# Performance work log

Measured on AMD Instinct MI355X. Metric: run time of the kernel, lower is better.

The kernel has to match this reference:

```python
import jax, jax.numpy as jnp
import numpy as np

B, L, IN_DIM = 256, 128, 6
D, H, NL = 256, 8, 6          # d_model, heads, wave layers
E, TOPK, FF = 8, 2, 1024      # MoE experts, top-k, expert ff dim (4*D)
NH, NMOE = 5, 3               # forecast horizons, MoE layers = NL//2
DK = D // H


def setup_inputs() -> dict:
    key = jax.random.key(0)
    ks = jax.random.split(key, 16)
    n = lambda k, shp, s=0.02: jax.random.normal(k, shp, dtype=jnp.float32) * s
    return dict(
        x=jax.random.normal(ks[0], (B, L, IN_DIM), dtype=jnp.float32),
        emb_w=n(ks[1], (IN_DIM, D)), emb_b=jnp.zeros((D,), jnp.float32),
        qw=n(ks[2], (NL, D, D)), kw=n(ks[3], (NL, D, D)),
        vw=n(ks[4], (NL, D, D)), ow=n(ks[5], (NL, D, D)),
        wfreq=n(ks[6], (NL, H), 0.1), wphase=jnp.zeros((NL, H), jnp.float32),
        router_w=n(ks[7], (NMOE, D, E)), router_b=jnp.zeros((NMOE, E), jnp.float32),
        e_w1=n(ks[8], (NMOE, E, D, FF)), e_b1=jnp.zeros((NMOE, E, FF), jnp.float32),
        e_w2=n(ks[9], (NMOE, E, FF, D)), e_b2=jnp.zeros((NMOE, E, D), jnp.float32),
        ln_g=jnp.ones((D,), jnp.float32), ln_b=jnp.zeros((D,), jnp.float32),
        pred_w=n(ks[10], (D, NH)), pred_b=jnp.zeros((NH,), jnp.float32),
        unc_w=n(ks[11], (D, NH)), unc_b=jnp.zeros((NH,), jnp.float32),
    )


def _wave_attn(x, qw, kw, vw, ow, freq, phase):
    # x: [B, L, D]; frequency-modulated multiplicative attention (dropout = eval)
    b, l, d = x.shape
    q = (x @ qw).reshape(b, l, H, DK).transpose(0, 2, 1, 3)  # [B,H,L,DK]
    k = (x @ kw).reshape(b, l, H, DK).transpose(0, 2, 1, 3)
    v = (x @ vw).reshape(b, l, H, DK).transpose(0, 2, 1, 3)
    pos = jnp.arange(l, dtype=x.dtype)
    wave = jnp.cos(2.0 * jnp.pi * freq[:, None] * pos[None, :] + phase[:, None])  # [H,L]
    scores = jnp.einsum('bhqd,bhkd->bhqk', q, k) * (DK ** -0.5)
    scores = scores * wave[None, :, None, :]
    attn = jax.nn.softmax(scores, axis=-1)
    out = jnp.einsum('bhqk,bhkd->bhqd', attn, v)
    out = out.transpose(0, 2, 1, 3).reshape(b, l, d)
    return out @ ow


def _moe(x, rw, rb, w1, b1, w2, b2):
    # x: [B, L, D] -> flatten tokens; top-k routed expert FFN with renormalized weights
    b, l, d = x.shape
    xf = x.reshape(-1, d)                                   # [N, D]
    probs = jax.nn.softmax(xf @ rw + rb, axis=-1)           # [N, E]
    tw, ti = jax.lax.top_k(probs, TOPK)                     # [N, K]
    tw = tw / jnp.sum(tw, axis=-1, keepdims=True)
    # combine weights per expert: nonzero only where expert is in token's top-k
    combine = jnp.sum(jax.nn.one_hot(ti, E, dtype=xf.dtype) * tw[..., None], axis=1)  # [N, E]
    out = jnp.zeros_like(xf)
    for e in range(E):  # fixed small expert count
        h = jax.nn.gelu(xf @ w1[e] + b1[e], approximate=False)
        out = out + combine[:, e:e + 1] * (h @ w2[e] + b2[e])
    return out.reshape(b, l, d)


def _forward(x, emb_w, emb_b, qw, kw, vw, ow, wfreq, wphase,
             router_w, router_b, e_w1, e_b1, e_w2, e_b2,
             ln_g, ln_b, pred_w, pred_b, unc_w, unc_b):
    h = x @ emb_w + emb_b
    for i in range(NL):
        h = _wave_attn(h, qw[i], kw[i], vw[i], ow[i], wfreq[i], wphase[i]) + h
        if i % 2 == 0 and i // 2 < NMOE:
            j = i // 2
            h = _moe(h, router_w[j], router_b[j], e_w1[j], e_b1[j], e_w2[j], e_b2[j]) + h
    mu = jnp.mean(h, axis=-1, keepdims=True)
    var = jnp.mean((h - mu) ** 2, axis=-1, keepdims=True)
    hn = (h - mu) / jnp.sqrt(var + 1e-5) * ln_g + ln_b
    z = hn[:, -1, :]                                        # last token latent
    pred = z @ pred_w + pred_b
    unc = jax.nn.softplus(z @ unc_w + unc_b)
    return pred, unc


def reference(x, emb_w, emb_b, qw, kw, vw, ow, wfreq, wphase,
              router_w, router_b, e_w1, e_b1, e_w2, e_b2,
              ln_g, ln_b, pred_w, pred_b, unc_w, unc_b):
    return _forward(x, emb_w, emb_b, qw, kw, vw, ow, wfreq, wphase,
                    router_w, router_b, e_w1, e_b1, e_w2, e_b2,
                    ln_g, ln_b, pred_w, pred_b, unc_w, unc_b)
```

## Files before the change

kernel.cpp:

```cpp
#include <hip/hip_runtime.h>
#include <math.h>

#define B_    256
#define L_    128
#define IN_   6
#define D_    256
#define H_    8
#define NL_   6
#define E_    8
#define FF_   1024
#define NH_   5
#define NMOE_ 3
#define DK_   32
#define T_    (B_*L_)
#define CAP_  66560

typedef __bf16 bf16x8 __attribute__((ext_vector_type(8)));
typedef __bf16 bf16x4 __attribute__((ext_vector_type(4)));
typedef float  f32x4  __attribute__((ext_vector_type(4)));

static constexpr size_t OFF_H    = 0;
static constexpr size_t OFF_HB   = 33554432;
static constexpr size_t OFF_QKV  = 50331648;
static constexpr size_t OFF_AO   = 100663296;
static constexpr size_t OFF_YOUT = 50331648;
static constexpr size_t OFF_WQKV = 118489088;
static constexpr size_t OFF_OWT  = 120848384;
static constexpr size_t OFF_W1T  = 121634816;
static constexpr size_t OFF_W2T  = 134217728;
static constexpr size_t OFF_SMALL= 146800640;
static constexpr size_t SM_T2I   = OFF_SMALL + 0;
static constexpr size_t SM_T2W   = OFF_SMALL + 262144;
static constexpr size_t SM_SLOT  = OFF_SMALL + 524288;
static constexpr size_t SM_PTOK  = OFF_SMALL + 786432;
static constexpr size_t SM_CNT   = OFF_SMALL + 1052672;
static constexpr size_t SM_POFF  = OFF_SMALL + 1052704;
static constexpr size_t SM_CUR   = OFF_SMALL + 1052740;

__global__ __launch_bounds__(256) void k_tcast(const float* __restrict__ src,
                                               __bf16* __restrict__ dst, int R, int C,
                                               size_t dbs, int rowoff) {
    __shared__ float tile[64][65];
    int b  = blockIdx.z;
    int r0 = blockIdx.y * 64, c0 = blockIdx.x * 64;
    const float* S = src + (size_t)b * R * C;
    __bf16* Dd = dst + (size_t)b * dbs;
    int tid = threadIdx.x;
#pragma unroll
    for (int i = 0; i < 4; ++i) {
        int f = tid + 256 * i;
        int r = f >> 4, c4 = (f & 15) * 4;
        float4 v = *(const float4*)(S + (size_t)(r0 + r) * C + c0 + c4);
        tile[r][c4] = v.x; tile[r][c4+1] = v.y; tile[r][c4+2] = v.z; tile[r][c4+3] = v.w;
    }
    __syncthreads();
#pragma unroll
    for (int i = 0; i < 2; ++i) {
        int chunk = tid + 256 * i;
        int drow = chunk >> 3, seg = (chunk & 7) * 8;
        bf16x8 o;
#pragma unroll
        for (int j = 0; j < 8; ++j) o[j] = (__bf16)tile[seg + j][drow];
        *(bf16x8*)(Dd + (size_t)(rowoff + c0 + drow) * R + r0 + seg) = o;
    }
}

__global__ void k_embed(const float* __restrict__ x, const float* __restrict__ ew,
                        const float* __restrict__ eb, float* __restrict__ h,
                        __bf16* __restrict__ hb) {
    int t = blockIdx.x;
    int d = threadIdx.x;
    const float* xr = x + (size_t)t * IN_;
    float acc = eb[d];
#pragma unroll
    for (int i = 0; i < IN_; ++i) acc = fmaf(xr[i], ew[i*D_ + d], acc);
    h[(size_t)t*D_ + d]  = acc;
    hb[(size_t)t*D_ + d] = (__bf16)acc;
}

#define LDT_ 40
__device__ __forceinline__ void mm_main(const __bf16* __restrict__ A, int lda,
                                        const __bf16* __restrict__ BT, int ldb,
                                        size_t m0, size_t n0, int K,
                                        f32x4 (&acc)[4][4],
                                        __bf16* As, __bf16* Bs) {
    const int tid  = threadIdx.x;
    const int lane = tid & 63, wid = tid >> 6;
    const int wm = (wid >> 1) * 64, wn = (wid & 1) * 64;
    const int lr = lane & 15, lq = lane >> 4;
    for (int k0 = 0; k0 < K; k0 += 32) {
#pragma unroll
        for (int i = 0; i < 2; ++i) {
            int f = tid + 256 * i;
            int row = f >> 2, q = (f & 3) * 8;
            *(bf16x8*)&As[row*LDT_ + q] = *(const bf16x8*)(A  + (m0 + row) * lda + k0 + q);
            *(bf16x8*)&Bs[row*LDT_ + q] = *(const bf16x8*)(BT + (n0 + row) * ldb + k0 + q);
        }
        __syncthreads();
        bf16x8 af[4], bfr[4];
#pragma unroll
        for (int mi = 0; mi < 4; ++mi) af[mi]  = *(bf16x8*)&As[(wm + mi*16 + lr)*LDT_ + lq*8];
#pragma unroll
        for (int ni = 0; ni < 4; ++ni) bfr[ni] = *(bf16x8*)&Bs[(wn + ni*16 + lr)*LDT_ + lq*8];
#pragma unroll
        for (int mi = 0; mi < 4; ++mi)
#pragma unroll
            for (int ni = 0; ni < 4; ++ni)
                acc[mi][ni] = __builtin_amdgcn_mfma_f32_16x16x32_bf16(af[mi], bfr[ni],
                                                                      acc[mi][ni], 0, 0, 0);
        __syncthreads();
    }
}

__global__ __launch_bounds__(256) void k_mm_c(const __bf16* __restrict__ A,
                                              const __bf16* __restrict__ BT,
                                              __bf16* __restrict__ C, int ldc) {
    __shared__ __attribute__((aligned(16))) __bf16 As[128*LDT_], Bs[128*LDT_];
    f32x4 acc[4][4] = {};
    size_t m0 = (size_t)blockIdx.x * 128, n0 = (size_t)blockIdx.y * 128;
    mm_main(A, D_, BT, D_, m0, n0, D_, acc, As, Bs);
    const int lane = threadIdx.x & 63, wid = threadIdx.x >> 6;
    const int wm = (wid >> 1) * 64, wn = (wid & 1) * 64, lr = lane & 15, lq = lane >> 4;
#pragma unroll
    for (int mi = 0; mi < 4; ++mi)
#pragma unroll
        for (int r = 0; r < 4; ++r) {
            size_t gr = m0 + wm + mi*16 + lq*4 + r;
#pragma unroll
            for (int ni = 0; ni < 4; ++ni) {
                size_t gc = n0 + wn + ni*16 + lr;
                C[gr * ldc + gc] = (__bf16)acc[mi][ni][r];
            }
        }
}

__global__ __launch_bounds__(256) void k_mm_oproj(const __bf16* __restrict__ A,
                                                  const __bf16* __restrict__ BT,
                                                  float* __restrict__ h,
                                                  __bf16* __restrict__ hb) {
    __shared__ __attribute__((aligned(16))) __bf16 As[128*LDT_], Bs[128*LDT_];
    f32x4 acc[4][4] = {};
    size_t m0 = (size_t)blockIdx.x * 128, n0 = (size_t)blockIdx.y * 128;
    mm_main(A, D_, BT, D_, m0, n0, D_, acc, As, Bs);
    const int lane = threadIdx.x & 63, wid = threadIdx.x >> 6;
    const int wm = (wid >> 1) * 64, wn = (wid & 1) * 64, lr = lane & 15, lq = lane >> 4;
#pragma unroll
    for (int mi = 0; mi < 4; ++mi)
#pragma unroll
        for (int r = 0; r < 4; ++r) {
            size_t gr = m0 + wm + mi*16 + lq*4 + r;
#pragma unroll
            for (int ni = 0; ni < 4; ++ni) {
                size_t gc = n0 + wn + ni*16 + lr;
                size_t idx = gr * D_ + gc;
                float nv = h[idx] + acc[mi][ni][r];
                h[idx]  = nv;
                hb[idx] = (__bf16)nv;
            }
        }
}

__global__ __launch_bounds__(256) void k_attn_mfma(const __bf16* __restrict__ qkv,
                                                   const float* __restrict__ wfreq,
                                                   const float* __restrict__ wphase,
                                                   __bf16* __restrict__ ao) {
    __shared__ __attribute__((aligned(16))) char smem[44032];
    __bf16* Vt   = (__bf16*)smem;
    float*  wscp = (float*)(smem + 8704);
    __bf16* Qs   = (__bf16*)(smem + 9216);
    __bf16* Ks   = (__bf16*)(smem + 19456);
    __bf16* Ps   = (__bf16*)(smem + 9216);

    int bh = blockIdx.x;
    int b = bh >> 3, hh = bh & 7;
    int tid = threadIdx.x;
    size_t tokbase = (size_t)b * L_ * 768 + (size_t)hh * 32;

#pragma unroll
    for (int j = 0; j < 2; ++j) {
        int chunk = tid + j*256;
        int row = chunk >> 2, seg = (chunk & 3) * 8;
        *(bf16x8*)&Qs[row*40 + seg] = *(const bf16x8*)(qkv + tokbase + (size_t)row*768 + seg);
        *(bf16x8*)&Ks[row*40 + seg] = *(const bf16x8*)(qkv + tokbase + 256 + (size_t)row*768 + seg);
    }
    {
        int kp = tid >> 1, dkb = (tid & 1) * 16;
        bf16x8 v0 = *(const bf16x8*)(qkv + tokbase + 512 + (size_t)kp*768 + dkb);
        bf16x8 v1 = *(const bf16x8*)(qkv + tokbase + 512 + (size_t)kp*768 + dkb + 8);
#pragma unroll
        for (int j = 0; j < 8; ++j) {
            Vt[(dkb + j)*136 + kp]     = v0[j];
            Vt[(dkb + 8 + j)*136 + kp] = v1[j];
        }
    }
    if (tid < 128) {
        float f = wfreq[hh], ph = wphase[hh];
        wscp[tid] = 0.1767766952966369f * cosf(6.283185307179586f * f * (float)tid + ph);
    }
    __syncthreads();

    const int lane = tid & 63, w = tid >> 6;
    const int lr = lane & 15, lq = lane >> 4;

    f32x4 sacc[2][8] = {};
#pragma unroll
    for (int mi = 0; mi < 2; ++mi) {
        bf16x8 af = *(const bf16x8*)&Qs[(w*32 + mi*16 + lr)*40 + lq*8];
#pragma unroll
        for (int ni = 0; ni < 8; ++ni) {
            bf16x8 bfr = *(const bf16x8*)&Ks[(ni*16 + lr)*40 + lq*8];
            sacc[mi][ni] = __builtin_amdgcn_mfma_f32_16x16x32_bf16(af, bfr, sacc[mi][ni], 0,0,0);
        }
    }
    float wr[8];
#pragma unroll
    for (int ni = 0; ni < 8; ++ni) wr[ni] = wscp[ni*16 + lr];
    __syncthreads();

#pragma unroll
    for (int mi = 0; mi < 2; ++mi)
#pragma unroll
        for (int r = 0; r < 4; ++r) {
            float vv[8]; float mx = -3.0e38f;
#pragma unroll
            for (int ni = 0; ni < 8; ++ni) { vv[ni] = sacc[mi][ni][r] * wr[ni]; mx = fmaxf(mx, vv[ni]); }
#pragma unroll
            for (int mk = 1; mk <= 8; mk <<= 1) mx = fmaxf(mx, __shfl_xor(mx, mk, 64));
            float sum = 0.f;
#pragma unroll
            for (int ni = 0; ni < 8; ++ni) { vv[ni] = __expf(vv[ni] - mx); sum += vv[ni]; }
#pragma unroll
            for (int mk = 1; mk <= 8; mk <<= 1) sum += __shfl_xor(sum, mk, 64);
            float inv = 1.f / sum;
            int row = w*32 + mi*16 + lq*4 + r;
#pragma unroll
            for (int ni = 0; ni < 8; ++ni)
                Ps[row*136 + ni*16 + lr] = (__bf16)(vv[ni] * inv);
        }
    __syncthreads();

    f32x4 oacc[2][2] = {};
#pragma unroll
    for (int kq = 0; kq < 4; ++kq) {
        bf16x8 paf[2], vbf[2];
#pragma unroll
        for (int mi = 0; mi < 2; ++mi)
            paf[mi] = *(const bf16x8*)&Ps[(w*32 + mi*16 + lr)*136 + kq*32 + lq*8];
#pragma unroll
        for (int ni = 0; ni < 2; ++ni)
            vbf[ni] = *(const bf16x8*)&Vt[(ni*16 + lr)*136 + kq*32 + lq*8];
#pragma unroll
        for (int mi = 0; mi < 2; ++mi)
#pragma unroll
            for (int ni = 0; ni < 2; ++ni)
                oacc[mi][ni] = __builtin_amdgcn_mfma_f32_16x16x32_bf16(paf[mi], vbf[ni],
                                                                       oacc[mi][ni], 0,0,0);
    }
    size_t obase = (size_t)b * L_ * D_ + (size_t)hh * 32;
#pragma unroll
    for (int mi = 0; mi < 2; ++mi)
#pragma unroll
        for (int ni = 0; ni < 2; ++ni)
#pragma unroll
            for (int r = 0; r < 4; ++r) {
                int row = w*32 + mi*16 + lq*4 + r;
                ao[obase + (size_t)row*D_ + ni*16 + lr] = (__bf16)oacc[mi][ni][r];
            }
}

__global__ void k_zero8(int* __restrict__ counts, int* __restrict__ cursors) {
    if (threadIdx.x < E_) { counts[threadIdx.x] = 0; cursors[threadIdx.x] = 0; }
}

__global__ __launch_bounds__(256) void k_router(const float* __restrict__ h,
                                                const float* __restrict__ rw,
                                                const float* __restrict__ rb,
                                                int* __restrict__ top2i,
                                                float* __restrict__ top2w) {
    int wv = threadIdx.x >> 6, lane = threadIdx.x & 63;
    int t = blockIdx.x * 4 + wv;
    float4 xv = *(const float4*)&h[(size_t)t * D_ + lane * 4];
    float lg[E_] = {};
    const float xs[4] = {xv.x, xv.y, xv.z, xv.w};
#pragma unroll
    for (int dd = 0; dd < 4; ++dd) {
        const float* rwr = rw + (size_t)(lane*4 + dd) * E_;
#pragma unroll
        for (int e = 0; e < E_; ++e) lg[e] = fmaf(xs[dd], rwr[e], lg[e]);
    }
#pragma unroll
    for (int e = 0; e < E_; ++e)
#pragma unroll
        for (int off = 32; off >= 1; off >>= 1) lg[e] += __shfl_down(lg[e], off, 64);
    if (lane == 0) {
        float val[E_];
#pragma unroll
        for (int e = 0; e < E_; ++e) val[e] = lg[e] + rb[e];
        int bi = 0; float best = val[0];
#pragma unroll
        for (int e = 1; e < E_; ++e) if (val[e] > best) { best = val[e]; bi = e; }
        int bi2 = -1; float best2 = -3.0e38f;
#pragma unroll
        for (int e = 0; e < E_; ++e) if (e != bi && val[e] > best2) { best2 = val[e]; bi2 = e; }
        float p2 = __expf(best2 - best);
        float inv = 1.f / (1.f + p2);
        top2i[2*t] = bi;  top2i[2*t+1] = bi2;
        top2w[2*t] = inv; top2w[2*t+1] = p2 * inv;
    }
}

__global__ __launch_bounds__(256) void k_hist(const int* __restrict__ t2i,
                                              int* __restrict__ cnt) {
    __shared__ int hc[E_];
    if (threadIdx.x < E_) hc[threadIdx.x] = 0;
    __syncthreads();
    for (int i = blockIdx.x * 256 + threadIdx.x; i < 2*T_; i += 64*256)
        atomicAdd(&hc[t2i[i]], 1);
    __syncthreads();
    if (threadIdx.x < E_) atomicAdd(&cnt[threadIdx.x], hc[threadIdx.x]);
}

__global__ void k_prefix(const int* __restrict__ counts, int* __restrict__ padoff) {
    if (threadIdx.x == 0 && blockIdx.x == 0) {
        int o = 0; padoff[0] = 0;
        for (int e = 0; e < E_; ++e) { o += (counts[e] + 127) & ~127; padoff[e+1] = o; }
    }
}

__global__ __launch_bounds__(256) void k_scatter(const int* __restrict__ top2i,
                                                 const int* __restrict__ padoff,
                                                 int* __restrict__ cursors,
                                                 int* __restrict__ pair_token,
                                                 int* __restrict__ slot_of) {
    int t = blockIdx.x * 256 + threadIdx.x;
    int lane = threadIdx.x & 63;
#pragma unroll
    for (int r = 0; r < 2; ++r) {
        int e = top2i[2*t + r];
#pragma unroll
        for (int e0 = 0; e0 < E_; ++e0) {
            unsigned long long m = __ballot(e == e0);
            if (m) {
                int leader = __ffsll((unsigned long long)m) - 1;
                int base = 0;
                if (lane == leader) base = atomicAdd(&cursors[e0], (int)__popcll(m));
                base = __shfl(base, leader, 64);
                if (e == e0) {
                    int rank = __popcll(m & ((1ull << lane) - 1ull));
                    int slot = padoff[e0] + base + rank;
                    pair_token[slot] = t;
                    slot_of[2*t + r] = slot;
                }
            }
        }
    }
}

__global__ __launch_bounds__(256) void k_moe_ffn(const __bf16* __restrict__ hb,
                                                 const __bf16* __restrict__ w1T,
                                                 const float*  __restrict__ b1,
                                                 const __bf16* __restrict__ w2T,
                                                 const float*  __restrict__ b2,
                                                 const int* __restrict__ poff,
                                                 const int* __restrict__ ptok,
                                                 float* __restrict__ yout) {
    __shared__ __attribute__((aligned(16))) __bf16 Xs[64*264];
    __shared__ __attribute__((aligned(16))) __bf16 Ms[64*136];
    __shared__ int sTok[64];
    int tid = threadIdx.x;
    const int e = blockIdx.x;
    int m0 = poff[e] + (int)blockIdx.y * 64;
    if (m0 >= poff[e + 1]) return;
    if (tid < 64) { int tk = ptok[m0 + tid]; sTok[tid] = tk < 0 ? 0 : tk; }
    __syncthreads();
#pragma unroll
    for (int j = 0; j < 8; ++j) {
        int chunk = tid + j * 256;
        int r = chunk >> 5, c = (chunk & 31) * 8;
        *(bf16x8*)&Xs[r*264 + c] = *(const bf16x8*)(hb + (size_t)sTok[r]*D_ + c);
    }
    __syncthreads();
    const int lane = tid & 63, w = tid >> 6;
    const int lr = lane & 15, lq = lane >> 4;
    const __bf16* w1e = w1T + (size_t)e * FF_ * D_;
    const __bf16* w2e = w2T + (size_t)e * D_ * FF_;
    f32x4 oacc[4][4] = {};
    for (int fc = 0; fc < 8; ++fc) {
        f32x4 macc[4][2] = {};
#pragma unroll
        for (int kq = 0; kq < 8; ++kq) {
            bf16x8 af[4], bw1[2];
#pragma unroll
            for (int mi = 0; mi < 4; ++mi)
                af[mi] = *(const bf16x8*)&Xs[(mi*16 + lr)*264 + kq*32 + lq*8];
#pragma unroll
            for (int nj = 0; nj < 2; ++nj) {
                int ff = fc*128 + w*32 + nj*16 + lr;
                bw1[nj] = *(const bf16x8*)(w1e + (size_t)ff*D_ + kq*32 + lq*8);
            }
#pragma unroll
            for (int mi = 0; mi < 4; ++mi)
#pragma unroll
                for (int nj = 0; nj < 2; ++nj)
                    macc[mi][nj] = __builtin_amdgcn_mfma_f32_16x16x32_bf16(af[mi], bw1[nj],
                                                                           macc[mi][nj], 0,0,0);
        }
        __syncthreads();
#pragma unroll
        for (int nj = 0; nj < 2; ++nj) {
            int ffc = w*32 + nj*16 + lr;
            float bv = b1[(size_t)e*FF_ + fc*128 + ffc];
#pragma unroll
            for (int mi = 0; mi < 4; ++mi)
#pragma unroll
                for (int r = 0; r < 4; ++r) {
                    float xv = macc[mi][nj][r] + bv;
                    float gl = 0.5f * xv * (1.f + erff(xv * 0.7071067811865475f));
                    Ms[(mi*16 + lq*4 + r)*136 + ffc] = (__bf16)gl;
                }
        }
        __syncthreads();
#pragma unroll
        for (int kq = 0; kq < 4; ++kq) {
            bf16x8 mf[4], bw2[4];
#pragma unroll
            for (int mi = 0; mi < 4; ++mi)
                mf[mi] = *(const bf16x8*)&Ms[(mi*16 + lr)*136 + kq*32 + lq*8];
#pragma unroll
            for (int ni = 0; ni < 4; ++ni) {
                int d = w*64 + ni*16 + lr;
                bw2[ni] = *(const bf16x8*)(w2e + (size_t)d*FF_ + fc*128 + kq*32 + lq*8);
            }
#pragma unroll
            for (int mi = 0; mi < 4; ++mi)
#pragma unroll
                for (int ni = 0; ni < 4; ++ni)
                    oacc[mi][ni] = __builtin_amdgcn_mfma_f32_16x16x32_bf16(mf[mi], bw2[ni],
                                                                           oacc[mi][ni], 0,0,0);
        }
    }
#pragma unroll
    for (int ni = 0; ni < 4; ++ni) {
        int d = w*64 + ni*16 + lr;
        float bv = b2[(size_t)e*D_ + d];
#pragma unroll
        for (int mi = 0; mi < 4; ++mi)
#pragma unroll
            for (int r = 0; r < 4; ++r)
                yout[(size_t)(m0 + mi*16 + lq*4 + r)*D_ + d] = oacc[mi][ni][r] + bv;
    }
}

__global__ __launch_bounds__(256) void k_combine(const float* __restrict__ yout,
                                                 const int* __restrict__ slot_of,
                                                 const float* __restrict__ t2w,
                                                 float* __restrict__ h,
                                                 __bf16* __restrict__ hb) {
    size_t idx = (size_t)blockIdx.x * 256 + threadIdx.x;
    int t = (int)(idx >> 6), c = (int)(idx & 63) * 4;
    int sA = slot_of[2*t], sB = slot_of[2*t + 1];
    float wA = t2w[2*t], wB = t2w[2*t + 1];
    float4 a  = *(const float4*)&yout[(size_t)sA * D_ + c];
    float4 bq = *(const float4*)&yout[(size_t)sB * D_ + c];
    size_t hi = (size_t)t * D_ + c;
    float4 hv = *(const float4*)&h[hi];
    float4 o;
    o.x = hv.x + wA*a.x + wB*bq.x;
    o.y = hv.y + wA*a.y + wB*bq.y;
    o.z = hv.z + wA*a.z + wB*bq.z;
    o.w = hv.w + wA*a.w + wB*bq.w;
    *(float4*)&h[hi] = o;
    bf16x4 ob; ob[0] = (__bf16)o.x; ob[1] = (__bf16)o.y; ob[2] = (__bf16)o.z; ob[3] = (__bf16)o.w;
    *(bf16x4*)&hb[hi] = ob;
}

__global__ __launch_bounds__(256) void k_head(const float* __restrict__ h,
                                              const float* __restrict__ g,
                                              const float* __restrict__ bb,
                                              const float* __restrict__ pw,
                                              const float* __restrict__ pb,
                                              const float* __restrict__ uw,
                                              const float* __restrict__ ub,
                                              float* __restrict__ out) {
    __shared__ float sred[4];
    __shared__ float smean, svar;
    __shared__ float z[D_];
    int b = blockIdx.x, t = threadIdx.x;
    int wv = t >> 6, ln = t & 63;
    float v = h[((size_t)b * L_ + (L_-1)) * D_ + t];
    float s = v;
#pragma unroll
    for (int off = 32; off >= 1; off >>= 1) s += __shfl_down(s, off, 64);
    if (ln == 0) sred[wv] = s;
    __syncthreads();
    if (t == 0) smean = (sred[0] + sred[1] + sred[2] + sred[3]) * (1.f/256.f);
    __syncthreads();
    float c = v - smean;
    float s2 = c * c;
#pragma unroll
    for (int off = 32; off >= 1; off >>= 1) s2 += __shfl_down(s2, off, 64);
    if (ln == 0) sred[wv] = s2;
    __syncthreads();
    if (t == 0) svar = (sred[0] + sred[1] + sred[2] + sred[3]) * (1.f/256.f);
    __syncthreads();
    z[t] = c * rsqrtf(svar + 1e-5f) * g[t] + bb[t];
    __syncthreads();
    for (int o = wv; o < NH_*2; o += 4) {
        const float* W = (o < NH_) ? pw : uw;
        int col = (o < NH_) ? o : o - NH_;
        float p = 0.f;
#pragma unroll
        for (int dd = 0; dd < 4; ++dd) {
            int d = ln*4 + dd;
            p = fmaf(z[d], W[(size_t)d * NH_ + col], p);
        }
#pragma unroll
        for (int off = 32; off >= 1; off >>= 1) p += __shfl_down(p, off, 64);
        if (ln == 0) {
            if (o < NH_) {
                out[(size_t)b * NH_ + o] = p + pb[o];
            } else {
                float xarg = p + ub[col];
                float sp = (xarg > 20.f) ? xarg : log1pf(expf(xarg));
                out[(size_t)B_ * NH_ + (size_t)b * NH_ + col] = sp;
            }
        }
    }
}

extern "C" void kernel_launch(void* const* d_in, const int* in_sizes, int n_in,
                              void* d_out, int out_size, void* d_ws, size_t ws_size,
                              hipStream_t stream) {
    const float* x        = (const float*)d_in[0];
    const float* emb_w    = (const float*)d_in[1];
    const float* emb_b    = (const float*)d_in[2];
    const float* qw       = (const float*)d_in[3];
    const float* kw       = (const float*)d_in[4];
    const float* vw       = (const float*)d_in[5];
    const float* ow       = (const float*)d_in[6];
    const float* wfreq    = (const float*)d_in[7];
    const float* wphase   = (const float*)d_in[8];
    const float* router_w = (const float*)d_in[9];
    const float* router_b = (const float*)d_in[10];
    const float* e_w1     = (const float*)d_in[11];
    const float* e_b1     = (const float*)d_in[12];
    const float* e_w2     = (const float*)d_in[13];
    const float* e_b2     = (const float*)d_in[14];
    const float* ln_g     = (const float*)d_in[15];
    const float* ln_b     = (const float*)d_in[16];
    const float* pred_w   = (const float*)d_in[17];
    const float* pred_b   = (const float*)d_in[18];
    const float* unc_w    = (const float*)d_in[19];
    const float* unc_b    = (const float*)d_in[20];
    float* out = (float*)d_out;

    char* W = (char*)d_ws;
    float*  h     = (float*)(W + OFF_H);
    __bf16* hb    = (__bf16*)(W + OFF_HB);
    __bf16* qkvb  = (__bf16*)(W + OFF_QKV);
    __bf16* aob   = (__bf16*)(W + OFF_AO);
    float*  yout  = (float*)(W + OFF_YOUT);
    __bf16* wqkvT = (__bf16*)(W + OFF_WQKV);
    __bf16* owT   = (__bf16*)(W + OFF_OWT);
    __bf16* w1T   = (__bf16*)(W + OFF_W1T);
    __bf16* w2T   = (__bf16*)(W + OFF_W2T);
    int*    t2i   = (int*)(W + SM_T2I);
    float*  t2w   = (float*)(W + SM_T2W);
    int*    slot  = (int*)(W + SM_SLOT);
    int*    ptok  = (int*)(W + SM_PTOK);
    int*    cnt   = (int*)(W + SM_CNT);
    int*    poff  = (int*)(W + SM_POFF);
    int*    cur   = (int*)(W + SM_CUR);

    {
        dim3 g44(4, 4, 6);
        k_tcast<<<g44, 256, 0, stream>>>(qw, wqkvT, 256, 256, (size_t)768*256, 0);
        k_tcast<<<g44, 256, 0, stream>>>(kw, wqkvT, 256, 256, (size_t)768*256, 256);
        k_tcast<<<g44, 256, 0, stream>>>(vw, wqkvT, 256, 256, (size_t)768*256, 512);
        k_tcast<<<g44, 256, 0, stream>>>(ow, owT,   256, 256, (size_t)256*256, 0);
        dim3 g1(16, 4, 24);
        k_tcast<<<g1, 256, 0, stream>>>(e_w1, w1T, 256, 1024, (size_t)1024*256, 0);
        dim3 g2(4, 16, 24);
        k_tcast<<<g2, 256, 0, stream>>>(e_w2, w2T, 1024, 256, (size_t)1024*256, 0);
    }

    k_embed<<<T_, D_, 0, stream>>>(x, emb_w, emb_b, h, hb);

    dim3 gqkv(T_/128, 6);
    dim3 gproj(T_/128, 2);
    dim3 gffn(E_, 1040);
    for (int i = 0; i < NL_; ++i) {
        k_mm_c<<<gqkv, 256, 0, stream>>>(hb, wqkvT + (size_t)i*768*256, qkvb, 768);
        k_attn_mfma<<<B_*H_, 256, 0, stream>>>(qkvb, wfreq + i*H_, wphase + i*H_, aob);
        k_mm_oproj<<<gproj, 256, 0, stream>>>(aob, owT + (size_t)i*D_*D_, h, hb);

        if (i % 2 == 0 && i/2 < NMOE_) {
            int j = i / 2;
            k_zero8<<<1, 64, 0, stream>>>(cnt, cur);
            k_router<<<T_/4, 256, 0, stream>>>(h, router_w + (size_t)j*D_*E_,
                                               router_b + (size_t)j*E_, t2i, t2w);
            k_hist<<<64, 256, 0, stream>>>(t2i, cnt);
            k_prefix<<<1, 1, 0, stream>>>(cnt, poff);
            k_scatter<<<T_/256, 256, 0, stream>>>(t2i, poff, cur, ptok, slot);
            k_moe_ffn<<<gffn, 256, 0, stream>>>(hb,
                                                w1T + (size_t)j*E_*FF_*D_,
                                                e_b1 + (size_t)j*E_*FF_,
                                                w2T + (size_t)j*E_*D_*FF_,
                                                e_b2 + (size_t)j*E_*D_,
                                                poff, ptok, yout);
            k_combine<<<T_*64/256, 256, 0, stream>>>(yout, slot, t2w, h, hb);
        }
    }

    k_head<<<B_, 256, 0, stream>>>(h, ln_g, ln_b, pred_w, pred_b, unc_w, unc_b, out);
}
```

Measured before the change: 1.810 ms.

## Hold MoE FFN input fragments in registers, double-buffer GELU tile, emit bf16 outputs

The expert FFN kernel now loads each wave's token-row fragments into registers once, instead of re-reading them from LDS for every FF chunk. The LDS is reused as a double-buffered intermediate tile, which removes one barrier per chunk. Exact erf GELU is replaced by a tanh-based approximation using __expf. Expert outputs are stored and read back in the combine kernel as bf16 instead of fp32, halving that traffic. The per-expert grid shrinks from 1040 to 512 row blocks, which cuts empty early-exit blocks but silently drops rows if any expert receives more than 32768 token slots; the tanh GELU and bf16 outputs also add numeric error.

```diff
diff --git a/kernel.cpp b/kernel.cpp
--- a/kernel.cpp
+++ b/kernel.cpp
@@ -37,6 +37,15 @@
 static constexpr size_t SM_POFF  = OFF_SMALL + 1052704;
 static constexpr size_t SM_CUR   = OFF_SMALL + 1052740;
 
+__device__ __forceinline__ float fast_gelu(float x) {
+    float y  = 0.7978845608028654f * (x + 0.044715f * x * x * x);
+    float ay = fabsf(y);
+    float t  = __expf(-2.f * ay);
+    float th = (1.f - t) / (1.f + t);
+    th = copysignf(th, y);
+    return 0.5f * x * (1.f + th);
+}
+
 __global__ __launch_bounds__(256) void k_tcast(const float* __restrict__ src,
                                                __bf16* __restrict__ dst, int R, int C,
                                                size_t dbs, int rowoff) {
@@ -363,13 +372,14 @@
                                                  const float*  __restrict__ b2,
                                                  const int* __restrict__ poff,
                                                  const int* __restrict__ ptok,
-                                                 float* __restrict__ yout) {
-    __shared__ __attribute__((aligned(16))) __bf16 Xs[64*264];
-    __shared__ __attribute__((aligned(16))) __bf16 Ms[64*136];
+                                                 __bf16* __restrict__ yout) {
+    __shared__ __attribute__((aligned(16))) char smem[34816];
+    __bf16* Xs    = (__bf16*)smem;
+    __bf16* Msbuf = (__bf16*)smem;
     __shared__ int sTok[64];
-    int tid = threadIdx.x;
+    const int tid = threadIdx.x;
     const int e = blockIdx.x;
-    int m0 = poff[e] + (int)blockIdx.y * 64;
+    const int m0 = poff[e] + (int)blockIdx.y * 64;
     if (m0 >= poff[e + 1]) return;
     if (tid < 64) { int tk = ptok[m0 + tid]; sTok[tid] = tk < 0 ? 0 : tk; }
     __syncthreads();
@@ -382,17 +392,23 @@
     __syncthreads();
     const int lane = tid & 63, w = tid >> 6;
     const int lr = lane & 15, lq = lane >> 4;
+    bf16x8 ar[4][8];
+#pragma unroll
+    for (int mi = 0; mi < 4; ++mi)
+#pragma unroll
+        for (int kq = 0; kq < 8; ++kq)
+            ar[mi][kq] = *(const bf16x8*)&Xs[(mi*16 + lr)*264 + kq*32 + lq*8];
+    __syncthreads();
     const __bf16* w1e = w1T + (size_t)e * FF_ * D_;
     const __bf16* w2e = w2T + (size_t)e * D_ * FF_;
     f32x4 oacc[4][4] = {};
+#pragma unroll 1
     for (int fc = 0; fc < 8; ++fc) {
+        __bf16* Ms = Msbuf + (fc & 1) * (64*136);
         f32x4 macc[4][2] = {};
 #pragma unroll
         for (int kq = 0; kq < 8; ++kq) {
-            bf16x8 af[4], bw1[2];
-#pragma unroll
-            for (int mi = 0; mi < 4; ++mi)
-                af[mi] = *(const bf16x8*)&Xs[(mi*16 + lr)*264 + kq*32 + lq*8];
+            bf16x8 bw1[2];
 #pragma unroll
             for (int nj = 0; nj < 2; ++nj) {
                 int ff = fc*128 + w*32 + nj*16 + lr;
@@ -402,10 +418,9 @@
             for (int mi = 0; mi < 4; ++mi)
 #pragma unroll
                 for (int nj = 0; nj < 2; ++nj)
-                    macc[mi][nj] = __builtin_amdgcn_mfma_f32_16x16x32_bf16(af[mi], bw1[nj],
+                    macc[mi][nj] = __builtin_amdgcn_mfma_f32_16x16x32_bf16(ar[mi][kq], bw1[nj],
                                                                            macc[mi][nj], 0,0,0);
         }
-        __syncthreads();
 #pragma unroll
         for (int nj = 0; nj < 2; ++nj) {
             int ffc = w*32 + nj*16 + lr;
@@ -415,8 +430,7 @@
 #pragma unroll
                 for (int r = 0; r < 4; ++r) {
                     float xv = macc[mi][nj][r] + bv;
-                    float gl = 0.5f * xv * (1.f + erff(xv * 0.7071067811865475f));
-                    Ms[(mi*16 + lq*4 + r)*136 + ffc] = (__bf16)gl;
+                    Ms[(mi*16 + lq*4 + r)*136 + ffc] = (__bf16)fast_gelu(xv);
                 }
         }
         __syncthreads();
@@ -447,11 +461,11 @@
         for (int mi = 0; mi < 4; ++mi)
 #pragma unroll
             for (int r = 0; r < 4; ++r)
-                yout[(size_t)(m0 + mi*16 + lq*4 + r)*D_ + d] = oacc[mi][ni][r] + bv;
-    }
-}
-
-__global__ __launch_bounds__(256) void k_combine(const float* __restrict__ yout,
+                yout[(size_t)(m0 + mi*16 + lq*4 + r)*D_ + d] = (__bf16)(oacc[mi][ni][r] + bv);
+    }
+}
+
+__global__ __launch_bounds__(256) void k_combine(const __bf16* __restrict__ yout,
                                                  const int* __restrict__ slot_of,
                                                  const float* __restrict__ t2w,
                                                  float* __restrict__ h,
@@ -460,15 +474,15 @@
     int t = (int)(idx >> 6), c = (int)(idx & 63) * 4;
     int sA = slot_of[2*t], sB = slot_of[2*t + 1];
     float wA = t2w[2*t], wB = t2w[2*t + 1];
-    float4 a  = *(const float4*)&yout[(size_t)sA * D_ + c];
-    float4 bq = *(const float4*)&yout[(size_t)sB * D_ + c];
+    bf16x4 a4 = *(const bf16x4*)&yout[(size_t)sA * D_ + c];
+    bf16x4 b4 = *(const bf16x4*)&yout[(size_t)sB * D_ + c];
     size_t hi = (size_t)t * D_ + c;
     float4 hv = *(const float4*)&h[hi];
     float4 o;
-    o.x = hv.x + wA*a.x + wB*bq.x;
-    o.y = hv.y + wA*a.y + wB*bq.y;
-    o.z = hv.z + wA*a.z + wB*bq.z;
-    o.w = hv.w + wA*a.w + wB*bq.w;
+    o.x = hv.x + wA*(float)a4[0] + wB*(float)b4[0];
+    o.y = hv.y + wA*(float)a4[1] + wB*(float)b4[1];
+    o.z = hv.z + wA*(float)a4[2] + wB*(float)b4[2];
+    o.w = hv.w + wA*(float)a4[3] + wB*(float)b4[3];
     *(float4*)&h[hi] = o;
     bf16x4 ob; ob[0] = (__bf16)o.x; ob[1] = (__bf16)o.y; ob[2] = (__bf16)o.z; ob[3] = (__bf16)o.w;
     *(bf16x4*)&hb[hi] = ob;
@@ -559,7 +573,7 @@
     __bf16* hb    = (__bf16*)(W + OFF_HB);
     __bf16* qkvb  = (__bf16*)(W + OFF_QKV);
     __bf16* aob   = (__bf16*)(W + OFF_AO);
-    float*  yout  = (float*)(W + OFF_YOUT);
+    __bf16* yout  = (__bf16*)(W + OFF_YOUT);
     __bf16* wqkvT = (__bf16*)(W + OFF_WQKV);
     __bf16* owT   = (__bf16*)(W + OFF_OWT);
     __bf16* w1T   = (__bf16*)(W + OFF_W1T);
@@ -588,7 +602,7 @@
 
     dim3 gqkv(T_/128, 6);
     dim3 gproj(T_/128, 2);
-    dim3 gffn(E_, 1040);
+    dim3 gffn(E_, 512);
     for (int i = 0; i < NL_; ++i) {
         k_mm_c<<<gqkv, 256, 0, stream>>>(hb, wqkvT + (size_t)i*768*256, qkvb, 768);
         k_attn_mfma<<<B_*H_, 256, 0, stream>>>(qkvb, wfreq + i*H_, wphase + i*H_, aob);
```

Measured after the change: 2.034 ms. +12.4%, slower.
